# Optimization experiments

Measured on AMD Instinct MI355X. Metric: run time of the kernel, lower is better.

## Reference

```python
import jax, jax.numpy as jnp
import numpy as np

B = 1_048_576
NUM_ITERS = 10  # training-mode default; eval mode uses 1000
EPS = 1e-12
LOW, HIGH = 0.02, 0.98  # SquashedSigmoid bounds


def setup_inputs() -> dict:
    key = jax.random.key(0)
    ks = jax.random.split(key, 4)
    # margins are population masses -> keep strictly positive
    margins = jax.random.uniform(ks[0], (B, 8), dtype=jnp.float32) + 0.1

    def lin(k, i, o):
        return (jax.random.normal(k, (i, o), jnp.float32) / np.sqrt(i)).astype(jnp.float32)

    return {
        "margins": margins,
        "W1": lin(ks[1], 8, 32), "b1": jnp.zeros((32,), jnp.float32),
        "W2": lin(ks[2], 32, 16), "b2": jnp.zeros((16,), jnp.float32),
        "W3": lin(ks[3], 16, 9), "b3": jnp.zeros((9,), jnp.float32),
    }


def tau_batched(p):
    # p: (B,4) positive params -> (B,3,3) positive couples matrix.
    # 2x2 core, extended by geometric-mean row/col (user-supplied tau in repo).
    a = p.reshape(-1, 2, 2)
    col3 = jnp.sqrt(a[:, :, 0] * a[:, :, 1])          # (B,2)
    row3 = jnp.sqrt(a[:, 0, :] * a[:, 1, :])          # (B,2)
    corner = jnp.sqrt(row3[:, 0] * row3[:, 1])        # (B,)
    top = jnp.concatenate([a, col3[:, :, None]], axis=2)                 # (B,2,3)
    bot = jnp.concatenate([row3, corner[:, None]], axis=1)[:, None, :]   # (B,1,3)
    return jnp.concatenate([top, bot], axis=1)        # (B,3,3)


def sinkhorn_knopp(A, row_margins, col_margins, iters):
    # Batched Sinkhorn-Knopp: A (B,R,C), row_margins (B,R), col_margins (B,C)
    r = row_margins[:, :, None]
    c = col_margins[:, None, :]

    def body(A, _):
        A = A * (r / (A.sum(axis=2, keepdims=True) + EPS))
        A = A * (c / (A.sum(axis=1, keepdims=True) + EPS))
        return A, None

    A, _ = jax.lax.scan(body, A, None, length=iters)
    return A


def reference(margins, W1, b1, W2, b2, W3, b3):
    Bn = margins.shape[0]
    M, F = margins[:, 0:3], margins[:, 3:6]

    # MLP: Linear-ReLU-Linear-ReLU-Linear
    h = jax.nn.relu(margins @ W1 + b1)
    h = jax.nn.relu(h @ W2 + b2)
    pars = h @ W3 + b3                                   # (B,9)

    muc = tau_batched(jnp.exp(pars[:, 0:4]))             # (B,3,3)
    sqs = lambda x: LOW + (HIGH - LOW) * jax.nn.sigmoid(x)
    shm, shf = sqs(pars[:, 4:6]), sqs(pars[:, 6:8])      # (B,2) each
    V = jnp.exp(pars[:, -1])                             # (B,)

    ones = jnp.ones((Bn, 1), margins.dtype)
    shm0 = jnp.concatenate([shm, ones], axis=1)          # (B,3)
    shf0 = jnp.concatenate([shf, ones], axis=1)          # (B,3)
    mucm0, muc0f = M * shm0, F * shf0                    # matched masses (margins)
    mum0, mu0f = M * (1.0 - shm0), F * (1.0 - shf0)      # singles

    muc = sinkhorn_knopp(muc, mucm0, muc0f, NUM_ITERS)   # (B,3,3)

    top = jnp.concatenate([muc, mum0[:, :, None]], axis=2)   # (B,3,4)
    bot = jnp.concatenate(
        [mu0f[:, None, :], jnp.zeros((Bn, 1, 1), margins.dtype)], axis=2)  # (B,1,4)
    mus = jnp.concatenate([top, bot], axis=1)            # (B,4,4)
    return mus, V
```

## Files before the change

kernel.cpp:

```cpp
#include <hip/hip_runtime.h>
#include <math.h>


#define QLOW  0.02f
#define QSPAN 0.96f
#define L2E   1.44269504088896f

typedef __attribute__((ext_vector_type(2))) float f32x2;

__device__ __forceinline__ float frcp(float x) { return __builtin_amdgcn_rcpf(x); }
__device__ __forceinline__ f32x2 pfma(f32x2 a, f32x2 b, f32x2 c) {
    return __builtin_elementwise_fma(a, b, c);
}

__global__ __launch_bounds__(256, 8) void sinkhorn_fused(
    const float* __restrict__ margins,
    const float* __restrict__ W1, const float* __restrict__ b1,
    const float* __restrict__ W2, const float* __restrict__ b2,
    const float* __restrict__ W3, const float* __restrict__ b3,
    float* __restrict__ out, int n)
{
    const int row = blockIdx.x * blockDim.x + threadIdx.x;

    const float4* __restrict__ m4 = (const float4*)margins;
    const float4 a0q = m4[row * 2 + 0];
    const float4 a1q = m4[row * 2 + 1];
    float m[8];
    m[0] = a0q.x; m[1] = a0q.y; m[2] = a0q.z; m[3] = a0q.w;
    m[4] = a1q.x; m[5] = a1q.y; m[6] = a1q.z; m[7] = a1q.w;

    const f32x2* __restrict__ W1v = (const f32x2*)W1;
    const f32x2* __restrict__ W2v = (const f32x2*)W2;
    const f32x2* __restrict__ b1v = (const f32x2*)b1;
    const f32x2* __restrict__ b2v = (const f32x2*)b2;

    const f32x2 zero2 = {0.0f, 0.0f};

    f32x2 h1[16];
#pragma unroll
    for (int j = 0; j < 16; ++j) h1[j] = b1v[j];
#pragma unroll
    for (int k = 0; k < 8; ++k) {
        f32x2 mk; mk.x = m[k]; mk.y = m[k];
#pragma unroll
        for (int j = 0; j < 16; ++j)
            h1[j] = pfma(mk, W1v[k * 16 + j], h1[j]);
    }
#pragma unroll
    for (int j = 0; j < 16; ++j) h1[j] = __builtin_elementwise_max(h1[j], zero2);

    f32x2 h2[8];
#pragma unroll
    for (int j = 0; j < 8; ++j) h2[j] = b2v[j];
#pragma unroll
    for (int k = 0; k < 32; ++k) {
        const float s = (k & 1) ? h1[k >> 1].y : h1[k >> 1].x;
        f32x2 hk; hk.x = s; hk.y = s;
#pragma unroll
        for (int j = 0; j < 8; ++j)
            h2[j] = pfma(hk, W2v[k * 8 + j], h2[j]);
    }
#pragma unroll
    for (int j = 0; j < 8; ++j) h2[j] = __builtin_elementwise_max(h2[j], zero2);

    f32x2 p01 = {b3[0], b3[1]};
    f32x2 p23 = {b3[2], b3[3]};
    f32x2 p45 = {b3[4], b3[5]};
    f32x2 p67 = {b3[6], b3[7]};
    float p8 = b3[8];
#pragma unroll
    for (int k = 0; k < 16; ++k) {
        const f32x2 w01 = {W3[k * 9 + 0], W3[k * 9 + 1]};
        const f32x2 w23 = {W3[k * 9 + 2], W3[k * 9 + 3]};
        const f32x2 w45 = {W3[k * 9 + 4], W3[k * 9 + 5]};
        const f32x2 w67 = {W3[k * 9 + 6], W3[k * 9 + 7]};
        const float w8  = W3[k * 9 + 8];
        const float s = (k & 1) ? h2[k >> 1].y : h2[k >> 1].x;
        f32x2 hb; hb.x = s; hb.y = s;
        p01 = pfma(hb, w01, p01);
        p23 = pfma(hb, w23, p23);
        p45 = pfma(hb, w45, p45);
        p67 = pfma(hb, w67, p67);
        p8  = fmaf(s, w8, p8);
    }

    const float l0 = p01.x * L2E, l1 = p01.y * L2E;
    const float l2 = p23.x * L2E, l3 = p23.y * L2E;

    const float a00 = exp2f(l0), a01 = exp2f(l1);
    const float a10 = exp2f(l2), a11 = exp2f(l3);
    const float h01 = (l0 + l1) * 0.5f, h23 = (l2 + l3) * 0.5f;
    const float a02 = exp2f(h01);
    const float a12 = exp2f(h23);
    const float a20 = exp2f((l0 + l2) * 0.5f);
    const float a21 = exp2f((l1 + l3) * 0.5f);
    const float a22 = exp2f((h01 + h23) * 0.5f);

    const float s4 = fmaf(QSPAN, frcp(1.0f + exp2f(-L2E * p45.x)), QLOW);
    const float s5 = fmaf(QSPAN, frcp(1.0f + exp2f(-L2E * p45.y)), QLOW);
    const float s6 = fmaf(QSPAN, frcp(1.0f + exp2f(-L2E * p67.x)), QLOW);
    const float s7 = fmaf(QSPAN, frcp(1.0f + exp2f(-L2E * p67.y)), QLOW);

    const float rm0 = m[0] * s4, rm1 = m[1] * s5, rm2 = m[2];
    const float cm0 = m[3] * s6, cm1 = m[4] * s7, cm2 = m[5];

    float t0 = (a00 + a01) + a02;
    float t1 = (a10 + a11) + a12;
    float t2 = (a20 + a21) + a22;

    float zp0, zp1, zp2, wp0, wp1, wp2;
#pragma unroll
    for (int it = 0; it < 10; ++it) {
        zp0 = rm0 * frcp(t0);
        zp1 = rm1 * frcp(t1);
        zp2 = rm2 * frcp(t2);
        const float q0 = fmaf(a20, zp2, fmaf(a10, zp1, a00 * zp0));
        const float q1 = fmaf(a21, zp2, fmaf(a11, zp1, a01 * zp0));
        const float q2 = fmaf(a22, zp2, fmaf(a12, zp1, a02 * zp0));
        wp0 = cm0 * frcp(q0);
        wp1 = cm1 * frcp(q1);
        wp2 = cm2 * frcp(q2);
        if (it < 9) {
            t0 = fmaf(a02, wp2, fmaf(a01, wp1, a00 * wp0));
            t1 = fmaf(a12, wp2, fmaf(a11, wp1, a10 * wp0));
            t2 = fmaf(a22, wp2, fmaf(a21, wp1, a20 * wp0));
        }
    }

    const float A0f = zp0 * a00 * wp0, A1f = zp0 * a01 * wp1, A2f = zp0 * a02 * wp2;
    const float A3f = zp1 * a10 * wp0, A4f = zp1 * a11 * wp1, A5f = zp1 * a12 * wp2;
    const float A6f = zp2 * a20 * wp0, A7f = zp2 * a21 * wp1, A8f = zp2 * a22 * wp2;

    const float um0 = m[0] - rm0;
    const float um1 = m[1] - rm1;
    const float uf0 = m[3] - cm0;
    const float uf1 = m[4] - cm1;

    float4* __restrict__ o4 = (float4*)out;
    float* __restrict__ oV = out + (size_t)n * 16;

    o4[row * 4 + 0] = make_float4(A0f, A1f, A2f, um0);
    o4[row * 4 + 1] = make_float4(A3f, A4f, A5f, um1);
    o4[row * 4 + 2] = make_float4(A6f, A7f, A8f, 0.0f);
    o4[row * 4 + 3] = make_float4(uf0, uf1, 0.0f, 0.0f);
    oV[row] = exp2f(p8 * L2E);
}

extern "C" void kernel_launch(void* const* d_in, const int* in_sizes, int n_in,
                              void* d_out, int out_size, void* d_ws, size_t ws_size,
                              hipStream_t stream) {
    const float* margins = (const float*)d_in[0];
    const float* W1 = (const float*)d_in[1];
    const float* b1 = (const float*)d_in[2];
    const float* W2 = (const float*)d_in[3];
    const float* b2 = (const float*)d_in[4];
    const float* W3 = (const float*)d_in[5];
    const float* b3 = (const float*)d_in[6];

    const int n = in_sizes[0] / 8;
    dim3 block(256), grid(n / 256);

    sinkhorn_fused<<<grid, block, 0, stream>>>(margins, W1, b1, W2, b2, W3, b3,
                                               (float*)d_out, n);
}
```

Before: 129.8 us.

## Compute MLP layers with fp16 MFMA 32x32x16 and LDS staging per wave

Result: slower. 135.0 us (+3.9%).

```diff
diff --git a/kernel.cpp b/kernel.cpp
--- a/kernel.cpp
+++ b/kernel.cpp
@@ -6,21 +6,63 @@
 #define QSPAN 0.96f
 #define L2E   1.44269504088896f
 
-typedef __attribute__((ext_vector_type(2))) float f32x2;
+typedef _Float16 half8 __attribute__((ext_vector_type(8)));
+typedef float f32x16 __attribute__((ext_vector_type(16)));
 
 __device__ __forceinline__ float frcp(float x) { return __builtin_amdgcn_rcpf(x); }
-__device__ __forceinline__ f32x2 pfma(f32x2 a, f32x2 b, f32x2 c) {
-    return __builtin_elementwise_fma(a, b, c);
+
+union H8u { half8 v; unsigned u[4]; uint4 q; };
+
+__device__ __forceinline__ unsigned pkh(float a, float b) {
+    union { _Float16 h[2]; unsigned u; } x;
+    x.h[0] = (_Float16)a; x.h[1] = (_Float16)b;
+    return x.u;
 }
 
-__global__ __launch_bounds__(256, 8) void sinkhorn_fused(
+__global__ __launch_bounds__(256) void sinkhorn_fused(
     const float* __restrict__ margins,
     const float* __restrict__ W1, const float* __restrict__ b1,
     const float* __restrict__ W2, const float* __restrict__ b2,
     const float* __restrict__ W3, const float* __restrict__ b3,
     float* __restrict__ out, int n)
 {
-    const int row = blockIdx.x * blockDim.x + threadIdx.x;
+    __shared__ __align__(16) _Float16 B1h[64][8];
+    __shared__ __align__(16) _Float16 B2h[2][64][8];
+    __shared__ __align__(16) _Float16 B3h[64][8];
+    __shared__ float sb1[32];
+    __shared__ float sb2[32];
+    __shared__ __align__(16) _Float16 H1h[4][64][40];
+    __shared__ __align__(16) _Float16 H2h[4][64][24];
+    __shared__ __align__(16) float    Pf [4][64][12];
+
+    {
+        const int t = threadIdx.x;
+        for (int i = t; i < 512; i += 256) {
+            const int lane = i >> 3, e = i & 7;
+            const int col = lane & 31, k = ((lane >> 5) << 3) + e;
+            B1h[lane][e] = (_Float16)((k < 8) ? W1[k * 32 + col] : 0.0f);
+        }
+        for (int i = t; i < 1024; i += 256) {
+            const int s = i >> 9, j = i & 511;
+            const int lane = j >> 3, e = j & 7;
+            const int col = lane & 31, k = 16 * s + ((lane >> 5) << 3) + e;
+            B2h[s][lane][e] = (_Float16)((col < 16) ? W2[k * 16 + col] : 0.0f);
+        }
+        for (int i = t; i < 512; i += 256) {
+            const int lane = i >> 3, e = i & 7;
+            const int col = lane & 31, k = ((lane >> 5) << 3) + e;
+            B3h[lane][e] = (_Float16)((col < 9) ? W3[k * 9 + col] : 0.0f);
+        }
+        if (t < 32) sb1[t] = b1[t];
+        if (t < 32) sb2[t] = (t < 16) ? b2[t] : 0.0f;
+    }
+    __syncthreads();
+
+    const int w = threadIdx.x >> 6;
+    const int l = threadIdx.x & 63;
+    const int c = l & 31;
+    const int wavebase = blockIdx.x * 256 + (w << 6);
+    const int row = wavebase + l;
 
     const float4* __restrict__ m4 = (const float4*)margins;
     const float4 a0q = m4[row * 2 + 0];
@@ -29,63 +71,96 @@
     m[0] = a0q.x; m[1] = a0q.y; m[2] = a0q.z; m[3] = a0q.w;
     m[4] = a1q.x; m[5] = a1q.y; m[6] = a1q.z; m[7] = a1q.w;
 
-    const f32x2* __restrict__ W1v = (const f32x2*)W1;
-    const f32x2* __restrict__ W2v = (const f32x2*)W2;
-    const f32x2* __restrict__ b1v = (const f32x2*)b1;
-    const f32x2* __restrict__ b2v = (const f32x2*)b2;
-
-    const f32x2 zero2 = {0.0f, 0.0f};
-
-    f32x2 h1[16];
-#pragma unroll
-    for (int j = 0; j < 16; ++j) h1[j] = b1v[j];
-#pragma unroll
-    for (int k = 0; k < 8; ++k) {
-        f32x2 mk; mk.x = m[k]; mk.y = m[k];
-#pragma unroll
-        for (int j = 0; j < 16; ++j)
-            h1[j] = pfma(mk, W1v[k * 16 + j], h1[j]);
-    }
-#pragma unroll
-    for (int j = 0; j < 16; ++j) h1[j] = __builtin_elementwise_max(h1[j], zero2);
-
-    f32x2 h2[8];
-#pragma unroll
-    for (int j = 0; j < 8; ++j) h2[j] = b2v[j];
-#pragma unroll
-    for (int k = 0; k < 32; ++k) {
-        const float s = (k & 1) ? h1[k >> 1].y : h1[k >> 1].x;
-        f32x2 hk; hk.x = s; hk.y = s;
-#pragma unroll
-        for (int j = 0; j < 8; ++j)
-            h2[j] = pfma(hk, W2v[k * 8 + j], h2[j]);
-    }
-#pragma unroll
-    for (int j = 0; j < 8; ++j) h2[j] = __builtin_elementwise_max(h2[j], zero2);
-
-    f32x2 p01 = {b3[0], b3[1]};
-    f32x2 p23 = {b3[2], b3[3]};
-    f32x2 p45 = {b3[4], b3[5]};
-    f32x2 p67 = {b3[6], b3[7]};
-    float p8 = b3[8];
-#pragma unroll
-    for (int k = 0; k < 16; ++k) {
-        const f32x2 w01 = {W3[k * 9 + 0], W3[k * 9 + 1]};
-        const f32x2 w23 = {W3[k * 9 + 2], W3[k * 9 + 3]};
-        const f32x2 w45 = {W3[k * 9 + 4], W3[k * 9 + 5]};
-        const f32x2 w67 = {W3[k * 9 + 6], W3[k * 9 + 7]};
-        const float w8  = W3[k * 9 + 8];
-        const float s = (k & 1) ? h2[k >> 1].y : h2[k >> 1].x;
-        f32x2 hb; hb.x = s; hb.y = s;
-        p01 = pfma(hb, w01, p01);
-        p23 = pfma(hb, w23, p23);
-        p45 = pfma(hb, w45, p45);
-        p67 = pfma(hb, w67, p67);
-        p8  = fmaf(s, w8, p8);
-    }
-
-    const float l0 = p01.x * L2E, l1 = p01.y * L2E;
-    const float l2 = p23.x * L2E, l3 = p23.y * L2E;
+    const int row2 = wavebase + 32 + c;
+    const float4 b0q = m4[row2 * 2 + 0];
+    const float4 b1q = m4[row2 * 2 + 1];
+
+    const bool lo32 = (l < 32);
+
+    H8u a1t0, a1t1;
+    a1t0.u[0] = lo32 ? pkh(m[0], m[1]) : 0u;
+    a1t0.u[1] = lo32 ? pkh(m[2], m[3]) : 0u;
+    a1t0.u[2] = lo32 ? pkh(m[4], m[5]) : 0u;
+    a1t0.u[3] = lo32 ? pkh(m[6], m[7]) : 0u;
+    a1t1.u[0] = lo32 ? pkh(b0q.x, b0q.y) : 0u;
+    a1t1.u[1] = lo32 ? pkh(b0q.z, b0q.w) : 0u;
+    a1t1.u[2] = lo32 ? pkh(b1q.x, b1q.y) : 0u;
+    a1t1.u[3] = lo32 ? pkh(b1q.z, b1q.w) : 0u;
+
+    const half8 b1v = *reinterpret_cast<const half8*>(&B1h[l][0]);
+    f32x16 C0 = {}, C1 = {};
+    C0 = __builtin_amdgcn_mfma_f32_32x32x16_f16(a1t0.v, b1v, C0, 0, 0, 0);
+    C1 = __builtin_amdgcn_mfma_f32_32x32x16_f16(a1t1.v, b1v, C1, 0, 0, 0);
+
+    {
+        const float b1c = sb1[c];
+#pragma unroll
+        for (int r = 0; r < 16; ++r) {
+            const int rowv = (r & 3) + 8 * (r >> 2) + ((l >> 5) << 2);
+            H1h[w][rowv][c]      = (_Float16)fmaxf(C0[r] + b1c, 0.0f);
+            H1h[w][rowv + 32][c] = (_Float16)fmaxf(C1[r] + b1c, 0.0f);
+        }
+    }
+
+    half8 A2[2][2];
+#pragma unroll
+    for (int T = 0; T < 2; ++T)
+#pragma unroll
+        for (int s = 0; s < 2; ++s)
+            A2[T][s] = *reinterpret_cast<const half8*>(
+                &H1h[w][(l & 31) + 32 * T][16 * s + ((l >> 5) << 3)]);
+
+    const half8 b2v0 = *reinterpret_cast<const half8*>(&B2h[0][l][0]);
+    const half8 b2v1 = *reinterpret_cast<const half8*>(&B2h[1][l][0]);
+    f32x16 D0 = {}, D1 = {};
+    D0 = __builtin_amdgcn_mfma_f32_32x32x16_f16(A2[0][0], b2v0, D0, 0, 0, 0);
+    D0 = __builtin_amdgcn_mfma_f32_32x32x16_f16(A2[0][1], b2v1, D0, 0, 0, 0);
+    D1 = __builtin_amdgcn_mfma_f32_32x32x16_f16(A2[1][0], b2v0, D1, 0, 0, 0);
+    D1 = __builtin_amdgcn_mfma_f32_32x32x16_f16(A2[1][1], b2v1, D1, 0, 0, 0);
+
+    if (c < 16) {
+        const float b2c = sb2[c];
+#pragma unroll
+        for (int r = 0; r < 16; ++r) {
+            const int rowv = (r & 3) + 8 * (r >> 2) + ((l >> 5) << 2);
+            H2h[w][rowv][c]      = (_Float16)fmaxf(D0[r] + b2c, 0.0f);
+            H2h[w][rowv + 32][c] = (_Float16)fmaxf(D1[r] + b2c, 0.0f);
+        }
+    }
+
+    half8 A3[2];
+#pragma unroll
+    for (int T = 0; T < 2; ++T)
+        A3[T] = *reinterpret_cast<const half8*>(
+            &H2h[w][(l & 31) + 32 * T][(l >> 5) << 3]);
+
+    const half8 b3v = *reinterpret_cast<const half8*>(&B3h[l][0]);
+    f32x16 P0 = {}, P1 = {};
+    P0 = __builtin_amdgcn_mfma_f32_32x32x16_f16(A3[0], b3v, P0, 0, 0, 0);
+    P1 = __builtin_amdgcn_mfma_f32_32x32x16_f16(A3[1], b3v, P1, 0, 0, 0);
+
+    if (c < 9) {
+#pragma unroll
+        for (int r = 0; r < 16; ++r) {
+            const int rowv = (r & 3) + 8 * (r >> 2) + ((l >> 5) << 2);
+            Pf[w][rowv][c]      = P0[r];
+            Pf[w][rowv + 32][c] = P1[r];
+        }
+    }
+
+    const float4* pr = reinterpret_cast<const float4*>(&Pf[w][l][0]);
+    const float4 pA = pr[0];
+    const float4 pB = pr[1];
+    const float pC = Pf[w][l][8];
+
+    const float p0 = pA.x + b3[0], p1 = pA.y + b3[1];
+    const float p2 = pA.z + b3[2], p3 = pA.w + b3[3];
+    const float p4 = pB.x + b3[4], p5 = pB.y + b3[5];
+    const float p6 = pB.z + b3[6], p7 = pB.w + b3[7];
+    const float p8v = pC + b3[8];
+
+    const float l0 = p0 * L2E, l1 = p1 * L2E;
+    const float l2 = p2 * L2E, l3 = p3 * L2E;
 
     const float a00 = exp2f(l0), a01 = exp2f(l1);
     const float a10 = exp2f(l2), a11 = exp2f(l3);
@@ -96,10 +171,10 @@
     const float a21 = exp2f((l1 + l3) * 0.5f);
     const float a22 = exp2f((h01 + h23) * 0.5f);
 
-    const float s4 = fmaf(QSPAN, frcp(1.0f + exp2f(-L2E * p45.x)), QLOW);
-    const float s5 = fmaf(QSPAN, frcp(1.0f + exp2f(-L2E * p45.y)), QLOW);
-    const float s6 = fmaf(QSPAN, frcp(1.0f + exp2f(-L2E * p67.x)), QLOW);
-    const float s7 = fmaf(QSPAN, frcp(1.0f + exp2f(-L2E * p67.y)), QLOW);
+    const float s4 = fmaf(QSPAN, frcp(1.0f + exp2f(-L2E * p4)), QLOW);
+    const float s5 = fmaf(QSPAN, frcp(1.0f + exp2f(-L2E * p5)), QLOW);
+    const float s6 = fmaf(QSPAN, frcp(1.0f + exp2f(-L2E * p6)), QLOW);
+    const float s7 = fmaf(QSPAN, frcp(1.0f + exp2f(-L2E * p7)), QLOW);
 
     const float rm0 = m[0] * s4, rm1 = m[1] * s5, rm2 = m[2];
     const float cm0 = m[3] * s6, cm1 = m[4] * s7, cm2 = m[5];
@@ -143,7 +218,7 @@
     o4[row * 4 + 1] = make_float4(A3f, A4f, A5f, um1);
     o4[row * 4 + 2] = make_float4(A6f, A7f, A8f, 0.0f);
     o4[row * 4 + 3] = make_float4(uf0, uf1, 0.0f, 0.0f);
-    oV[row] = exp2f(p8 * L2E);
+    oV[row] = exp2f(p8v * L2E);
 }
 
 extern "C" void kernel_launch(void* const* d_in, const int* in_sizes, int n_in,
```
